# Optimization experiments

Hardware: AMD Instinct MI355X
Metric: run time of the kernel (lower is better)

## Reference

```python
import jax, jax.numpy as jnp
import numpy as np
import math

D_MODEL = 512
H = 8
DK = D_MODEL // H  # 64
DFF = 2048
EPS = 1e-5


def layernorm(x, g, b):
    mu = jnp.mean(x, axis=-1, keepdims=True)
    var = jnp.mean((x - mu) ** 2, axis=-1, keepdims=True)
    return (x - mu) * jax.lax.rsqrt(var + EPS) * g + b


def gelu(x):
    return jax.nn.gelu(x, approximate=False)  # torch nn.GELU default (erf)


def feedforward(x, W1, b1, lng, lnb, W2, b2):
    x1 = jnp.einsum('btd,df->btf', x, W1) + b1
    x1 = gelu(layernorm(x1, lng, lnb))
    return jnp.einsum('btf,fd->btd', x1, W2) + b2


def setup_inputs() -> dict:
    key = jax.random.key(0)
    ks = iter(jax.random.split(key, 32))
    s = 0.02
    d = {}
    d['x'] = jax.random.normal(next(ks), (4, 2048, D_MODEL), jnp.float32)
    # per-head QKV projections, stacked over heads: [H, d_model, dk]
    d['Wq'] = jax.random.normal(next(ks), (H, D_MODEL, DK), jnp.float32) * s
    d['bq'] = jnp.zeros((H, DK), jnp.float32)
    d['Wk'] = jax.random.normal(next(ks), (H, D_MODEL, DK), jnp.float32) * s
    d['bk'] = jnp.zeros((H, DK), jnp.float32)
    d['Wv'] = jax.random.normal(next(ks), (H, D_MODEL, DK), jnp.float32) * s
    d['bv'] = jnp.zeros((H, DK), jnp.float32)
    d['Wo'] = jax.random.normal(next(ks), (D_MODEL, D_MODEL), jnp.float32) * s
    d['bo'] = jnp.zeros((D_MODEL,), jnp.float32)
    d['ln1_g'] = jnp.ones((D_MODEL,), jnp.float32)
    d['ln1_b'] = jnp.zeros((D_MODEL,), jnp.float32)
    # main FFN
    d['ff_W1'] = jax.random.normal(next(ks), (D_MODEL, DFF), jnp.float32) * s
    d['ff_b1'] = jnp.zeros((DFF,), jnp.float32)
    d['ff_lng'] = jnp.ones((DFF,), jnp.float32)
    d['ff_lnb'] = jnp.zeros((DFF,), jnp.float32)
    d['ff_W2'] = jax.random.normal(next(ks), (DFF, D_MODEL), jnp.float32) * s
    d['ff_b2'] = jnp.zeros((D_MODEL,), jnp.float32)
    d['ln2_g'] = jnp.ones((D_MODEL,), jnp.float32)
    d['ln2_b'] = jnp.zeros((D_MODEL,), jnp.float32)
    d['alphaA'] = jnp.zeros((1,), jnp.float32) + 0.1
    d['alphaB'] = jnp.zeros((1,), jnp.float32) + 0.1
    d['p1'] = jnp.asarray(0.1, jnp.float32)
    # sub1 FFN
    d['s1_W1'] = jax.random.normal(next(ks), (D_MODEL, DFF), jnp.float32) * s
    d['s1_b1'] = jnp.zeros((DFF,), jnp.float32)
    d['s1_lng'] = jnp.ones((DFF,), jnp.float32)
    d['s1_lnb'] = jnp.zeros((DFF,), jnp.float32)
    d['s1_W2'] = jax.random.normal(next(ks), (DFF, D_MODEL), jnp.float32) * s
    d['s1_b2'] = jnp.zeros((D_MODEL,), jnp.float32)
    d['lnsub1_g'] = jnp.ones((D_MODEL,), jnp.float32)
    d['lnsub1_b'] = jnp.zeros((D_MODEL,), jnp.float32)
    d['p2'] = jnp.asarray(0.1, jnp.float32)
    d['sub2_W'] = jax.random.normal(next(ks), (D_MODEL, D_MODEL), jnp.float32) * s
    d['sub2_b'] = jnp.zeros((D_MODEL,), jnp.float32)
    d['lnsub2_g'] = jnp.ones((D_MODEL,), jnp.float32)
    d['lnsub2_b'] = jnp.zeros((D_MODEL,), jnp.float32)
    return d


def reference(x, Wq, bq, Wk, bk, Wv, bv, Wo, bo, ln1_g, ln1_b,
              ff_W1, ff_b1, ff_lng, ff_lnb, ff_W2, ff_b2, ln2_g, ln2_b,
              alphaA, alphaB, p1, s1_W1, s1_b1, s1_lng, s1_lnb, s1_W2, s1_b2,
              lnsub1_g, lnsub1_b, p2, sub2_W, sub2_b, lnsub2_g, lnsub2_b):
    # --- multi-head attention (q = k = v = x) ---
    q = jnp.einsum('btd,hdk->bhtk', x, Wq) + bq[:, None, :]
    k = jnp.einsum('btd,hdk->bhtk', x, Wk) + bk[:, None, :]
    v = jnp.einsum('btd,hdk->bhtk', x, Wv) + bv[:, None, :]
    scores = jnp.einsum('bhtk,bhsk->bhts', q, k) / math.sqrt(DK)
    probs = jax.nn.softmax(scores, axis=-1)
    heads = jnp.einsum('bhts,bhsv->bhtv', probs, v)           # [B,H,T,dv]
    B, _, T, _ = heads.shape
    cat = jnp.transpose(heads, (0, 2, 1, 3)).reshape(B, T, H * DK)
    attn = jnp.einsum('btd,de->bte', cat, Wo) + bo
    # --- residual stack ---
    ln1 = layernorm(x + attn, ln1_g, ln1_b)
    out1 = x + ln1 * alphaA
    fft = feedforward(out1, ff_W1, ff_b1, ff_lng, ff_lnb, ff_W2, ff_b2)
    ln2 = layernorm(fft + out1, ln2_g, ln2_b)
    out2 = out1 + ln2 * alphaB
    # --- sub-branch 1 ---
    sub1 = feedforward(x, s1_W1, s1_b1, s1_lng, s1_lnb, s1_W2, s1_b2)
    sub1 = p1 * gelu(layernorm(sub1, lnsub1_g, lnsub1_b))
    # --- sub-branch 2 ---
    sub2 = jnp.einsum('btd,de->bte', x, sub2_W) + sub2_b
    sub2 = p2 * gelu(layernorm(sub2, lnsub2_g, lnsub2_b))
    return out2 + sub1 + sub2
```

## Files before the change

kernel.cpp:

```cpp
#include <hip/hip_runtime.h>
#include <hip/hip_bf16.h>
#include <math.h>

typedef __hip_bfloat16 bf16;
typedef __attribute__((ext_vector_type(8))) short s8v;
typedef __attribute__((ext_vector_type(4))) float f4v;

#define T_SEQ 2048
#define ROWS 8192
#define DMODEL 512
#define DFF 2048
#define QS 2048

#define GL2LDS(g, l) __builtin_amdgcn_global_load_lds( \
    (const __attribute__((address_space(1))) void*)(g), \
    (__attribute__((address_space(3))) void*)(l), 16, 0, 0)

__device__ __forceinline__ float b2f(bf16 v) { return __bfloat162float(v); }
__device__ __forceinline__ bf16 f2b(float v) { return __float2bfloat16(v); }
__device__ __forceinline__ float us2f(unsigned short u) {
    union { float f; unsigned int u; } c; c.u = ((unsigned int)u) << 16; return c.f;
}
__device__ __forceinline__ unsigned short f2us(float v) {
    bf16 b = f2b(v); return *(unsigned short*)&b;
}
__device__ __forceinline__ float gelu_f(float x) {
    return 0.5f * x * (1.0f + erff(x * 0.70710678118654752440f));
}
__device__ __forceinline__ float ldP(const void* p, int i, bool f32) {
    return f32 ? ((const float*)p)[i] : b2f(((const bf16*)p)[i]);
}

__global__ __launch_bounds__(256) void sniff_kernel(const void* __restrict__ x,
                                                    int* __restrict__ flag) {
    __shared__ float red[4];
    int tid = threadIdx.x;
    const bf16* p = (const bf16*)x;
    float mx = 0.f;
    for (int i = tid; i < 65536; i += 256) {
        float v = b2f(p[i]);
        if (!(v == v)) v = 1e30f;
        mx = fmaxf(mx, fabsf(v));
    }
    #pragma unroll
    for (int o = 32; o; o >>= 1) mx = fmaxf(mx, __shfl_down(mx, o));
    if ((tid & 63) == 0) red[tid >> 6] = mx;
    __syncthreads();
    if (tid == 0) {
        float m = fmaxf(fmaxf(red[0], red[1]), fmaxf(red[2], red[3]));
        flag[0] = (m > 1000.f) ? 1 : 0;
    }
}

__global__ __launch_bounds__(256) void cvt_b16(const void* __restrict__ in,
                                               unsigned short* __restrict__ out, int n,
                                               const int* __restrict__ flag) {
    bool f32 = flag[0] != 0;
    int i = blockIdx.x * 256 + threadIdx.x;
    if (i < n) out[i] = f2us(ldP(in, i, f32));
}

#define WBIG_E 1048576
__global__ __launch_bounds__(256) void repack_all(const void* Wq, const void* Wk, const void* Wv,
                                                  const void* s2W, const void* ffW1, const void* ffW2,
                                                  const void* s1W1, const void* s1W2, const void* Wo,
                                                  unsigned short* __restrict__ Wbig,
                                                  unsigned short* __restrict__ ffW1t,
                                                  unsigned short* __restrict__ ffW2t,
                                                  unsigned short* __restrict__ s1W1t,
                                                  unsigned short* __restrict__ s1W2t,
                                                  unsigned short* __restrict__ Wot,
                                                  const int* __restrict__ flag) {
    bool f32 = flag[0] != 0;
    int idx = blockIdx.x * 256 + threadIdx.x;
    if (idx < WBIG_E) {
        int n = idx >> 9, d = idx & 511;
        float v;
        if (n < 1536) {
            int sec = n >> 9, nn = n & 511;
            int h = nn >> 6, j = nn & 63;
            const void* W = sec == 0 ? Wq : (sec == 1 ? Wk : Wv);
            v = ldP(W, (h * 512 + d) * 64 + j, f32);
        } else {
            v = ldP(s2W, d * 512 + (n - 1536), f32);
        }
        Wbig[idx] = f2us(v);
    } else if (idx < 2 * WBIG_E) {
        int i2 = idx - WBIG_E;
        int n = i2 >> 9, kd = i2 & 511;
        ffW1t[i2] = f2us(ldP(ffW1, kd * 2048 + n, f32));
    } else if (idx < 3 * WBIG_E) {
        int i2 = idx - 2 * WBIG_E;
        int n = i2 >> 11, kd = i2 & 2047;
        ffW2t[i2] = f2us(ldP(ffW2, kd * 512 + n, f32));
    } else if (idx < 4 * WBIG_E) {
        int i2 = idx - 3 * WBIG_E;
        int n = i2 >> 9, kd = i2 & 511;
        s1W1t[i2] = f2us(ldP(s1W1, kd * 2048 + n, f32));
    } else if (idx < 5 * WBIG_E) {
        int i2 = idx - 4 * WBIG_E;
        int n = i2 >> 11, kd = i2 & 2047;
        s1W2t[i2] = f2us(ldP(s1W2, kd * 512 + n, f32));
    } else if (idx < 5 * WBIG_E + 262144) {
        int i2 = idx - 5 * WBIG_E;
        int n = i2 >> 9, kd = i2 & 511;
        Wot[i2] = f2us(ldP(Wo, kd * 512 + n, f32));
    }
}

__global__ __launch_bounds__(256) void bias_fuse(const void* bq, const void* bk, const void* bv,
                                                 const void* s2b, const void* bo, const void* ffb1,
                                                 const void* ffb2, const void* s1b1, const void* s1b2,
                                                 float* __restrict__ out,
                                                 const int* __restrict__ flag) {
    bool f32 = flag[0] != 0;
    int i = blockIdx.x * 256 + threadIdx.x;
    if (i >= 7680) return;
    const void* src; int off;
    if      (i < 512)  { src = bq;   off = i; }
    else if (i < 1024) { src = bk;   off = i - 512; }
    else if (i < 1536) { src = bv;   off = i - 1024; }
    else if (i < 2048) { src = s2b;  off = i - 1536; }
    else if (i < 2560) { src = bo;   off = i - 2048; }
    else if (i < 4608) { src = ffb1; off = i - 2560; }
    else if (i < 5120) { src = ffb2; off = i - 4608; }
    else if (i < 7168) { src = s1b1; off = i - 5120; }
    else               { src = s1b2; off = i - 7168; }
    out[i] = ldP(src, off, f32);
}

__global__ __launch_bounds__(256) void gemm_mfma(const unsigned short* __restrict__ A,
                                                 const unsigned short* __restrict__ Bt,
                                                 const float* __restrict__ bias,
                                                 void* __restrict__ C0,
                                                 void* __restrict__ C1,
                                                 int M, int N, int K, int kLen,
                                                 int outBf16) {
    __shared__ unsigned short As[128 * 64];
    __shared__ unsigned short Bs[128 * 64];
    int tid = threadIdx.x;
    int wave = tid >> 6, lane = tid & 63;
    int wm = wave >> 1, wn = wave & 1;
    int quad = lane >> 4, l16 = lane & 15;
    int bm = blockIdx.y * 128, bn = blockIdx.x * 128;
    int z = blockIdx.z;
    int kOff = z * kLen;
    f4v acc[4][4] = {};
    int rsub = lane >> 3;
    int kcst = lane & 7;
    for (int k0 = kOff; k0 < kOff + kLen; k0 += 64) {
        #pragma unroll
        for (int i = 0; i < 4; i++) {
            int rowT = wave * 32 + i * 8 + rsub;
            int kc = (kcst - rowT) & 7;
            GL2LDS(A + (size_t)(bm + rowT) * K + k0 + kc * 8,
                   &As[(wave * 32 + i * 8) * 64]);
            GL2LDS(Bt + (size_t)(bn + rowT) * K + k0 + kc * 8,
                   &Bs[(wave * 32 + i * 8) * 64]);
        }
        __syncthreads();
        #pragma unroll
        for (int ks = 0; ks < 64; ks += 32) {
            int kchunk = (ks >> 3) + quad;
            s8v af[4], bfr[4];
            #pragma unroll
            for (int mi = 0; mi < 4; mi++) {
                int m = wm * 64 + mi * 16 + l16;
                af[mi] = *(const s8v*)&As[m * 64 + (((kchunk + m) & 7) * 8)];
            }
            #pragma unroll
            for (int ni = 0; ni < 4; ni++) {
                int n = wn * 64 + ni * 16 + l16;
                bfr[ni] = *(const s8v*)&Bs[n * 64 + (((kchunk + n) & 7) * 8)];
            }
            #pragma unroll
            for (int mi = 0; mi < 4; mi++)
                #pragma unroll
                for (int ni = 0; ni < 4; ni++)
                    acc[mi][ni] = __builtin_amdgcn_mfma_f32_16x16x32_bf16(
                        af[mi], bfr[ni], acc[mi][ni], 0, 0, 0);
        }
        __syncthreads();
    }
    bool doBias = (z == 0);
    float bcol[4];
    #pragma unroll
    for (int ni = 0; ni < 4; ni++)
        bcol[ni] = doBias ? bias[bn + wn * 64 + ni * 16 + l16] : 0.f;
    void* Cd = z ? C1 : C0;
    #pragma unroll
    for (int mi = 0; mi < 4; mi++) {
        #pragma unroll
        for (int rg = 0; rg < 4; rg++) {
            size_t row = bm + wm * 64 + mi * 16 + quad * 4 + rg;
            #pragma unroll
            for (int ni = 0; ni < 4; ni++) {
                int col = bn + wn * 64 + ni * 16 + l16;
                float v = acc[mi][ni][rg] + bcol[ni];
                if (outBf16) ((unsigned short*)Cd)[row * N + col] = f2us(v);
                else         ((float*)Cd)[row * N + col] = v;
            }
        }
    }
}

__global__ __launch_bounds__(256) void transpose_v(const unsigned short* __restrict__ QKV,
                                                   unsigned short* __restrict__ Vt) {
    __shared__ unsigned short tile[64][72];
    int kt = blockIdx.x;
    int bh = blockIdx.y;
    int b = bh >> 3, h = bh & 7;
    const unsigned short* Vg = QKV + ((size_t)b * T_SEQ) * QS + 1024 + h * 64;
    int tid = threadIdx.x;
    int r = tid >> 3, c = (tid & 7) * 8;
    #pragma unroll
    for (int it = 0; it < 2; it++) {
        int rr = r + it * 32;
        uint4 v = *(const uint4*)(Vg + (size_t)(kt * 64 + rr) * QS + c);
        *(uint4*)&tile[rr][c] = v;
    }
    __syncthreads();
    #pragma unroll
    for (int it = 0; it < 2; it++) {
        int d = r + it * 32;
        unsigned short tmp[8];
        #pragma unroll
        for (int j = 0; j < 8; j++) tmp[j] = tile[c + j][d];
        *(uint4*)(Vt + ((size_t)(bh * 64 + d)) * T_SEQ + kt * 64 + c) = *(uint4*)tmp;
    }
}

#define ALD 72
#define SCL2 0.18033688f
__global__ __launch_bounds__(256) void attn_mfma(const unsigned short* __restrict__ QKV,
                                                 const unsigned short* __restrict__ Vt,
                                                 unsigned short* __restrict__ O) {
    __shared__ unsigned short Qs[64 * ALD];
    __shared__ unsigned short Ks[64 * ALD];
    __shared__ unsigned short Vts[64 * ALD];
    __shared__ unsigned short Ps[64 * ALD];

    int tid = threadIdx.x;
    int wave = tid >> 6, lane = tid & 63;
    int quad = lane >> 4, l16 = lane & 15;
    int qbase = blockIdx.x * 64;
    int bh = blockIdx.y;
    int b = bh >> 3, h = bh & 7;
    const unsigned short* Qg = QKV + ((size_t)(b * T_SEQ + qbase)) * QS + h * 64;
    const unsigned short* Kg = QKV + ((size_t)b * T_SEQ) * QS + 512 + h * 64;
    const unsigned short* Vtg = Vt + (size_t)bh * 64 * T_SEQ;

    int r = tid >> 3, c = (tid & 7) * 8;
    #pragma unroll
    for (int it = 0; it < 2; it++) {
        int rr = r + it * 32;
        uint4 v = *(const uint4*)(Qg + (size_t)rr * QS + c);
        *(uint4*)&Qs[rr * ALD + c] = v;
    }
    float lrun[4] = {0.f, 0.f, 0.f, 0.f};
    f4v oacc[4] = {};
    __syncthreads();

    for (int kt = 0; kt < 32; ++kt) {
        #pragma unroll
        for (int it = 0; it < 2; it++) {
            int rr = r + it * 32;
            uint4 kv = *(const uint4*)(Kg + (size_t)(kt * 64 + rr) * QS + c);
            *(uint4*)&Ks[rr * ALD + c] = kv;
            uint4 vv = *(const uint4*)(Vtg + (size_t)rr * T_SEQ + kt * 64 + c);
            *(uint4*)&Vts[rr * ALD + c] = vv;
        }
        __syncthreads();

        f4v sacc[4] = {};
        #pragma unroll
        for (int kc2 = 0; kc2 < 2; kc2++) {
            s8v aq = *(const s8v*)&Qs[(wave * 16 + l16) * ALD + kc2 * 32 + quad * 8];
            #pragma unroll
            for (int ni = 0; ni < 4; ni++) {
                s8v bk_ = *(const s8v*)&Ks[(ni * 16 + l16) * ALD + kc2 * 32 + quad * 8];
                sacc[ni] = __builtin_amdgcn_mfma_f32_16x16x32_bf16(aq, bk_, sacc[ni], 0, 0, 0);
            }
        }
        #pragma unroll
        for (int rg = 0; rg < 4; rg++) {
            #pragma unroll
            for (int ni = 0; ni < 4; ni++) {
                float p = exp2f(fminf(sacc[ni][rg] * SCL2, 30.f));
                lrun[rg] += p;
                Ps[(wave * 16 + quad * 4 + rg) * ALD + ni * 16 + l16] = f2us(p);
            }
        }
        #pragma unroll
        for (int kc2 = 0; kc2 < 2; kc2++) {
            s8v ap = *(const s8v*)&Ps[(wave * 16 + l16) * ALD + kc2 * 32 + quad * 8];
            #pragma unroll
            for (int ni = 0; ni < 4; ni++) {
                s8v bv_ = *(const s8v*)&Vts[(ni * 16 + l16) * ALD + kc2 * 32 + quad * 8];
                oacc[ni] = __builtin_amdgcn_mfma_f32_16x16x32_bf16(ap, bv_, oacc[ni], 0, 0, 0);
            }
        }
        __syncthreads();
    }

    #pragma unroll
    for (int rg = 0; rg < 4; rg++) {
        float l = lrun[rg];
        #pragma unroll
        for (int o = 8; o; o >>= 1) l += __shfl_xor(l, o);
        float linv = 1.0f / l;
        size_t orow = ((size_t)(b * T_SEQ + qbase + wave * 16 + quad * 4 + rg)) * 512 + h * 64;
        #pragma unroll
        for (int ni = 0; ni < 4; ni++)
            O[orow + ni * 16 + l16] = f2us(oacc[ni][rg] * linv);
    }
}

__global__ __launch_bounds__(256) void ln_residual(const void* __restrict__ Xraw,
                                                   const float* __restrict__ Y,
                                                   const float* __restrict__ Y2,
                                                   const float* __restrict__ Xf,
                                                   const void* __restrict__ g,
                                                   const void* __restrict__ bb,
                                                   const void* __restrict__ alpha,
                                                   float* __restrict__ out,
                                                   unsigned short* __restrict__ outb,
                                                   const int* __restrict__ flag) {
    __shared__ float red[8];
    bool f32 = flag[0] != 0;
    int row = blockIdx.x, tid = threadIdx.x;
    size_t base = (size_t)row * DMODEL;
    float x0 = Xraw ? ldP(Xraw, base + tid, f32) : Xf[base + tid];
    float x1 = Xraw ? ldP(Xraw, base + tid + 256, f32) : Xf[base + tid + 256];
    float v0 = x0 + Y[base + tid];
    float v1 = x1 + Y[base + tid + 256];
    if (Y2) { v0 += Y2[base + tid]; v1 += Y2[base + tid + 256]; }
    float s = v0 + v1, s2 = v0 * v0 + v1 * v1;
    #pragma unroll
    for (int o = 32; o; o >>= 1) { s += __shfl_down(s, o); s2 += __shfl_down(s2, o); }
    if ((tid & 63) == 0) { red[tid >> 6] = s; red[4 + (tid >> 6)] = s2; }
    __syncthreads();
    s = red[0] + red[1] + red[2] + red[3];
    s2 = red[4] + red[5] + red[6] + red[7];
    float mu = s * (1.0f / 512.0f);
    float var = s2 * (1.0f / 512.0f) - mu * mu;
    float rr = rsqrtf(var + 1e-5f);
    float a = ldP(alpha, 0, f32);
    float o0 = x0 + a * ((v0 - mu) * rr * ldP(g, tid, f32) + ldP(bb, tid, f32));
    float o1 = x1 + a * ((v1 - mu) * rr * ldP(g, tid + 256, f32) + ldP(bb, tid + 256, f32));
    out[base + tid] = o0;
    out[base + tid + 256] = o1;
    if (outb) {
        outb[base + tid] = f2us(o0);
        outb[base + tid + 256] = f2us(o1);
    }
}

__global__ __launch_bounds__(256) void ln_gelu(unsigned short* __restrict__ Hm,
                                               const void* __restrict__ g,
                                               const void* __restrict__ bb,
                                               const int* __restrict__ flag) {
    __shared__ float red[8];
    bool f32 = flag[0] != 0;
    int row = blockIdx.x, tid = threadIdx.x;
    size_t base = (size_t)row * DFF;
    float v[8];
    float s = 0.f, s2 = 0.f;
    #pragma unroll
    for (int i = 0; i < 8; i++) {
        v[i] = us2f(Hm[base + tid + i * 256]);
        s += v[i]; s2 += v[i] * v[i];
    }
    #pragma unroll
    for (int o = 32; o; o >>= 1) { s += __shfl_down(s, o); s2 += __shfl_down(s2, o); }
    if ((tid & 63) == 0) { red[tid >> 6] = s; red[4 + (tid >> 6)] = s2; }
    __syncthreads();
    s = red[0] + red[1] + red[2] + red[3];
    s2 = red[4] + red[5] + red[6] + red[7];
    float mu = s * (1.0f / 2048.0f);
    float var = s2 * (1.0f / 2048.0f) - mu * mu;
    float r = rsqrtf(var + 1e-5f);
    #pragma unroll
    for (int i = 0; i < 8; i++) {
        int cc = tid + i * 256;
        float ln = (v[i] - mu) * r * ldP(g, cc, f32) + ldP(bb, cc, f32);
        Hm[base + cc] = f2us(gelu_f(ln));
    }
}

__global__ __launch_bounds__(256) void final_kernel(const float* __restrict__ O2,
                                                    const float* __restrict__ S1,
                                                    const float* __restrict__ S1b,
                                                    const unsigned short* __restrict__ S2,
                                                    const void* __restrict__ g1,
                                                    const void* __restrict__ b1,
                                                    const void* __restrict__ g2,
                                                    const void* __restrict__ b2,
                                                    const void* __restrict__ p1,
                                                    const void* __restrict__ p2,
                                                    void* __restrict__ out,
                                                    const int* __restrict__ flag) {
    __shared__ float red[16];
    bool f32 = flag[0] != 0;
    int row = blockIdx.x, tid = threadIdx.x;
    size_t base = (size_t)row * DMODEL;
    size_t base2 = (size_t)row * QS;
    float a0 = S1[base + tid] + S1b[base + tid];
    float a1 = S1[base + tid + 256] + S1b[base + tid + 256];
    float c0 = us2f(S2[base2 + tid]);
    float c1 = us2f(S2[base2 + tid + 256]);
    float sa = a0 + a1, sa2 = a0 * a0 + a1 * a1;
    float sc = c0 + c1, sc2 = c0 * c0 + c1 * c1;
    #pragma unroll
    for (int o = 32; o; o >>= 1) {
        sa += __shfl_down(sa, o); sa2 += __shfl_down(sa2, o);
        sc += __shfl_down(sc, o); sc2 += __shfl_down(sc2, o);
    }
    int w = tid >> 6;
    if ((tid & 63) == 0) { red[w] = sa; red[4 + w] = sa2; red[8 + w] = sc; red[12 + w] = sc2; }
    __syncthreads();
    sa = red[0] + red[1] + red[2] + red[3];
    sa2 = red[4] + red[5] + red[6] + red[7];
    sc = red[8] + red[9] + red[10] + red[11];
    sc2 = red[12] + red[13] + red[14] + red[15];
    float mua = sa * (1.0f / 512.0f), vara = sa2 * (1.0f / 512.0f) - mua * mua;
    float ra = rsqrtf(vara + 1e-5f);
    float muc = sc * (1.0f / 512.0f), varc = sc2 * (1.0f / 512.0f) - muc * muc;
    float rc = rsqrtf(varc + 1e-5f);
    float fp1 = ldP(p1, 0, f32), fp2 = ldP(p2, 0, f32);
    float av[2] = {a0, a1}, cv[2] = {c0, c1};
    #pragma unroll
    for (int i = 0; i < 2; i++) {
        int cc = tid + i * 256;
        float l1 = (av[i] - mua) * ra * ldP(g1, cc, f32) + ldP(b1, cc, f32);
        float l2 = (cv[i] - muc) * rc * ldP(g2, cc, f32) + ldP(b2, cc, f32);
        float o = O2[base + cc] + fp1 * gelu_f(l1) + fp2 * gelu_f(l2);
        if (f32) ((float*)out)[base + cc] = o;
        else     ((bf16*)out)[base + cc] = f2b(o);
    }
}

extern "C" void kernel_launch(void* const* d_in, const int* in_sizes, int n_in,
                              void* d_out, int out_size, void* d_ws, size_t ws_size,
                              hipStream_t stream) {
    (void)in_sizes; (void)n_in; (void)out_size; (void)ws_size;
    const void* x      = d_in[0];
    const void* Wq     = d_in[1];
    const void* bq     = d_in[2];
    const void* Wk     = d_in[3];
    const void* bk     = d_in[4];
    const void* Wv     = d_in[5];
    const void* bv     = d_in[6];
    const void* Wo     = d_in[7];
    const void* bo     = d_in[8];
    const void* ln1_g  = d_in[9];
    const void* ln1_b  = d_in[10];
    const void* ffW1   = d_in[11];
    const void* ffb1   = d_in[12];
    const void* fflng  = d_in[13];
    const void* fflnb  = d_in[14];
    const void* ffW2   = d_in[15];
    const void* ffb2   = d_in[16];
    const void* ln2_g  = d_in[17];
    const void* ln2_b  = d_in[18];
    const void* alphaA = d_in[19];
    const void* alphaB = d_in[20];
    const void* p1     = d_in[21];
    const void* s1W1   = d_in[22];
    const void* s1b1   = d_in[23];
    const void* s1lng  = d_in[24];
    const void* s1lnb  = d_in[25];
    const void* s1W2   = d_in[26];
    const void* s1b2   = d_in[27];
    const void* lns1g  = d_in[28];
    const void* lns1b  = d_in[29];
    const void* p2     = d_in[30];
    const void* s2W    = d_in[31];
    const void* s2b    = d_in[32];
    const void* lns2g  = d_in[33];
    const void* lns2b  = d_in[34];

    char* base = (char*)d_ws;
    size_t off = 0;
    auto alloc = [&](size_t bytes) {
        char* p = base + off;
        off += (bytes + 255) & ~(size_t)255;
        return p;
    };
    int* flag            = (int*)alloc(64);
    unsigned short* Wbig  = (unsigned short*)alloc((size_t)2048 * 512 * 2);
    unsigned short* Wot   = (unsigned short*)alloc(512 * 512 * 2);
    unsigned short* ffW1t = (unsigned short*)alloc((size_t)2048 * 512 * 2);
    unsigned short* ffW2t = (unsigned short*)alloc((size_t)512 * 2048 * 2);
    unsigned short* s1W1t = (unsigned short*)alloc((size_t)2048 * 512 * 2);
    unsigned short* s1W2t = (unsigned short*)alloc((size_t)512 * 2048 * 2);
    float* bias_all       = (float*)alloc(7680 * 4);
    unsigned short* xb    = (unsigned short*)alloc((size_t)ROWS * 512 * 2);
    unsigned short* Cbig  = (unsigned short*)alloc((size_t)ROWS * QS * 2);
    unsigned short* h1    = (unsigned short*)alloc((size_t)ROWS * DFF * 2);
    unsigned short* Vtb   = (unsigned short*)alloc((size_t)ROWS * 512 * 2);
    char*  regionC        = alloc((size_t)ROWS * 512 * 2);
    char*  regionB        = alloc((size_t)ROWS * 512 * 4);
    char*  regionD        = alloc((size_t)ROWS * 512 * 4);
    float* out2           = (float*)alloc((size_t)ROWS * 512 * 4);

    float* attn           = (float*)regionB;
    float* fft            = (float*)regionB;
    float* sub1raw2       = (float*)regionB;
    unsigned short* catb  = (unsigned short*)regionC;
    unsigned short* out1b = (unsigned short*)regionC;
    float* out1           = (float*)regionD;
    float* sub1raw        = (float*)regionD;
    float* attn2          = out2;
    float* fft2           = out2;

    float* biasBig = bias_all + 0;
    float* biasWo  = bias_all + 2048;
    float* biasF1  = bias_all + 2560;
    float* biasF2  = bias_all + 4608;
    float* biasS11 = bias_all + 5120;
    float* biasS12 = bias_all + 7168;

    sniff_kernel<<<1, 256, 0, stream>>>(x, flag);
    cvt_b16<<<(ROWS * 512 + 255) / 256, 256, 0, stream>>>(x, xb, ROWS * 512, flag);
    repack_all<<<(5 * WBIG_E + 262144 + 255) / 256, 256, 0, stream>>>(
        Wq, Wk, Wv, s2W, ffW1, ffW2, s1W1, s1W2, Wo,
        Wbig, ffW1t, ffW2t, s1W1t, s1W2t, Wot, flag);
    bias_fuse<<<30, 256, 0, stream>>>(bq, bk, bv, s2b, bo, ffb1, ffb2, s1b1, s1b2,
                                      bias_all, flag);

    auto gemm = [&](const unsigned short* A, const unsigned short* Bt, const float* bias,
                    void* C0, void* C1, int M, int N, int K, int outBf16, int split) {
        int kLen = split ? K / 2 : K;
        gemm_mfma<<<dim3(N / 128, M / 128, split ? 2 : 1), 256, 0, stream>>>(
            A, Bt, bias, C0, C1, M, N, K, kLen, outBf16);
    };

    gemm(xb, Wbig, biasBig, Cbig, nullptr, ROWS, QS, 512, 1, 0);
    transpose_v<<<dim3(32, 32), 256, 0, stream>>>(Cbig, Vtb);
    attn_mfma<<<dim3(T_SEQ / 64, 32), 256, 0, stream>>>(Cbig, Vtb, catb);
    gemm(catb, Wot, biasWo, attn, attn2, ROWS, 512, 512, 0, 1);
    ln_residual<<<ROWS, 256, 0, stream>>>(x, attn, attn2, nullptr,
                                          ln1_g, ln1_b, alphaA, out1, out1b, flag);
    gemm(out1b, ffW1t, biasF1, h1, nullptr, ROWS, DFF, 512, 1, 0);
    ln_gelu<<<ROWS, 256, 0, stream>>>(h1, fflng, fflnb, flag);
    gemm(h1, ffW2t, biasF2, fft, fft2, ROWS, 512, DFF, 0, 1);
    ln_residual<<<ROWS, 256, 0, stream>>>(nullptr, fft, fft2, out1,
                                          ln2_g, ln2_b, alphaB, out2,
                                          (unsigned short*)nullptr, flag);
    gemm(xb, s1W1t, biasS11, h1, nullptr, ROWS, DFF, 512, 1, 0);
    ln_gelu<<<ROWS, 256, 0, stream>>>(h1, s1lng, s1lnb, flag);
    gemm(h1, s1W2t, biasS12, sub1raw, sub1raw2, ROWS, 512, DFF, 0, 1);
    final_kernel<<<ROWS, 256, 0, stream>>>(out2, sub1raw, sub1raw2, Cbig + 1536,
                                           lns1g, lns1b, lns2g, lns2b,
                                           p1, p2, d_out, flag);
}
```

Measured before the change: 559.6 us.

## Fuse sub1 first-layer GEMM into QKV projection and store split-K partials as bf16

The sub-branch-1 first FFN weight is appended to the big QKV+sub2 weight, so one wider GEMM over x produces Q, K, V, sub2 and the sub1 hidden activations together. The GEMM gains lda/ldc strides so later GEMMs and ln_gelu can read and write the hidden slice inside the wide buffer in place. The sub1 branch is then processed early, the attention-output and sub1 split-K partials are written as bf16 instead of fp32, and buffers are re-aliased. The aim is fewer launches, better GEMM occupancy and less memory traffic, at the cost of extra bf16 rounding in the partial sums and more complex buffer aliasing.

After: 558.8 us. Within noise of the previous version (-0.2%).

```diff
diff --git a/kernel.cpp b/kernel.cpp
--- a/kernel.cpp
+++ b/kernel.cpp
@@ -10,7 +10,7 @@
 #define ROWS 8192
 #define DMODEL 512
 #define DFF 2048
-#define QS 2048
+#define QS 4096
 
 #define GL2LDS(g, l) __builtin_amdgcn_global_load_lds( \
     (const __attribute__((address_space(1))) void*)(g), \
@@ -60,20 +60,19 @@
     if (i < n) out[i] = f2us(ldP(in, i, f32));
 }
 
-#define WBIG_E 1048576
 __global__ __launch_bounds__(256) void repack_all(const void* Wq, const void* Wk, const void* Wv,
-                                                  const void* s2W, const void* ffW1, const void* ffW2,
-                                                  const void* s1W1, const void* s1W2, const void* Wo,
-                                                  unsigned short* __restrict__ Wbig,
+                                                  const void* s2W, const void* s1W1,
+                                                  const void* ffW1, const void* ffW2,
+                                                  const void* s1W2, const void* Wo,
+                                                  unsigned short* __restrict__ Wbig2,
                                                   unsigned short* __restrict__ ffW1t,
                                                   unsigned short* __restrict__ ffW2t,
-                                                  unsigned short* __restrict__ s1W1t,
                                                   unsigned short* __restrict__ s1W2t,
                                                   unsigned short* __restrict__ Wot,
                                                   const int* __restrict__ flag) {
     bool f32 = flag[0] != 0;
     int idx = blockIdx.x * 256 + threadIdx.x;
-    if (idx < WBIG_E) {
+    if (idx < 2097152) {
         int n = idx >> 9, d = idx & 511;
         float v;
         if (n < 1536) {
@@ -81,36 +80,34 @@
             int h = nn >> 6, j = nn & 63;
             const void* W = sec == 0 ? Wq : (sec == 1 ? Wk : Wv);
             v = ldP(W, (h * 512 + d) * 64 + j, f32);
+        } else if (n < 2048) {
+            v = ldP(s2W, d * 512 + (n - 1536), f32);
         } else {
-            v = ldP(s2W, d * 512 + (n - 1536), f32);
-        }
-        Wbig[idx] = f2us(v);
-    } else if (idx < 2 * WBIG_E) {
-        int i2 = idx - WBIG_E;
+            v = ldP(s1W1, d * 2048 + (n - 2048), f32);
+        }
+        Wbig2[idx] = f2us(v);
+    } else if (idx < 3145728) {
+        int i2 = idx - 2097152;
         int n = i2 >> 9, kd = i2 & 511;
         ffW1t[i2] = f2us(ldP(ffW1, kd * 2048 + n, f32));
-    } else if (idx < 3 * WBIG_E) {
-        int i2 = idx - 2 * WBIG_E;
+    } else if (idx < 4194304) {
+        int i2 = idx - 3145728;
         int n = i2 >> 11, kd = i2 & 2047;
         ffW2t[i2] = f2us(ldP(ffW2, kd * 512 + n, f32));
-    } else if (idx < 4 * WBIG_E) {
-        int i2 = idx - 3 * WBIG_E;
-        int n = i2 >> 9, kd = i2 & 511;
-        s1W1t[i2] = f2us(ldP(s1W1, kd * 2048 + n, f32));
-    } else if (idx < 5 * WBIG_E) {
-        int i2 = idx - 4 * WBIG_E;
+    } else if (idx < 5242880) {
+        int i2 = idx - 4194304;
         int n = i2 >> 11, kd = i2 & 2047;
         s1W2t[i2] = f2us(ldP(s1W2, kd * 512 + n, f32));
-    } else if (idx < 5 * WBIG_E + 262144) {
-        int i2 = idx - 5 * WBIG_E;
+    } else if (idx < 5505024) {
+        int i2 = idx - 5242880;
         int n = i2 >> 9, kd = i2 & 511;
         Wot[i2] = f2us(ldP(Wo, kd * 512 + n, f32));
     }
 }
 
 __global__ __launch_bounds__(256) void bias_fuse(const void* bq, const void* bk, const void* bv,
-                                                 const void* s2b, const void* bo, const void* ffb1,
-                                                 const void* ffb2, const void* s1b1, const void* s1b2,
+                                                 const void* s2b, const void* s1b1, const void* bo,
+                                                 const void* ffb1, const void* ffb2, const void* s1b2,
                                                  float* __restrict__ out,
                                                  const int* __restrict__ flag) {
     bool f32 = flag[0] != 0;
@@ -121,20 +118,20 @@
     else if (i < 1024) { src = bk;   off = i - 512; }
     else if (i < 1536) { src = bv;   off = i - 1024; }
     else if (i < 2048) { src = s2b;  off = i - 1536; }
-    else if (i < 2560) { src = bo;   off = i - 2048; }
-    else if (i < 4608) { src = ffb1; off = i - 2560; }
-    else if (i < 5120) { src = ffb2; off = i - 4608; }
-    else if (i < 7168) { src = s1b1; off = i - 5120; }
+    else if (i < 4096) { src = s1b1; off = i - 2048; }
+    else if (i < 4608) { src = bo;   off = i - 4096; }
+    else if (i < 6656) { src = ffb1; off = i - 4608; }
+    else if (i < 7168) { src = ffb2; off = i - 6656; }
     else               { src = s1b2; off = i - 7168; }
     out[i] = ldP(src, off, f32);
 }
 
-__global__ __launch_bounds__(256) void gemm_mfma(const unsigned short* __restrict__ A,
+__global__ __launch_bounds__(256) void gemm_mfma(const unsigned short* __restrict__ A, int lda,
                                                  const unsigned short* __restrict__ Bt,
                                                  const float* __restrict__ bias,
                                                  void* __restrict__ C0,
                                                  void* __restrict__ C1,
-                                                 int M, int N, int K, int kLen,
+                                                 int M, int N, int ldc, int K, int kLen,
                                                  int outBf16) {
     __shared__ unsigned short As[128 * 64];
     __shared__ unsigned short Bs[128 * 64];
@@ -153,7 +150,7 @@
         for (int i = 0; i < 4; i++) {
             int rowT = wave * 32 + i * 8 + rsub;
             int kc = (kcst - rowT) & 7;
-            GL2LDS(A + (size_t)(bm + rowT) * K + k0 + kc * 8,
+            GL2LDS(A + (size_t)(bm + rowT) * lda + k0 + kc * 8,
                    &As[(wave * 32 + i * 8) * 64]);
             GL2LDS(Bt + (size_t)(bn + rowT) * K + k0 + kc * 8,
                    &Bs[(wave * 32 + i * 8) * 64]);
@@ -197,8 +194,8 @@
             for (int ni = 0; ni < 4; ni++) {
                 int col = bn + wn * 64 + ni * 16 + l16;
                 float v = acc[mi][ni][rg] + bcol[ni];
-                if (outBf16) ((unsigned short*)Cd)[row * N + col] = f2us(v);
-                else         ((float*)Cd)[row * N + col] = v;
+                if (outBf16) ((unsigned short*)Cd)[row * ldc + col] = f2us(v);
+                else         ((float*)Cd)[row * ldc + col] = v;
             }
         }
     }
@@ -316,25 +313,23 @@
     }
 }
 
-__global__ __launch_bounds__(256) void ln_residual(const void* __restrict__ Xraw,
-                                                   const float* __restrict__ Y,
-                                                   const float* __restrict__ Y2,
-                                                   const float* __restrict__ Xf,
-                                                   const void* __restrict__ g,
-                                                   const void* __restrict__ bb,
-                                                   const void* __restrict__ alpha,
-                                                   float* __restrict__ out,
-                                                   unsigned short* __restrict__ outb,
-                                                   const int* __restrict__ flag) {
+__global__ __launch_bounds__(256) void ln_res1(const void* __restrict__ Xraw,
+                                               const unsigned short* __restrict__ Ya,
+                                               const unsigned short* __restrict__ Yb,
+                                               const void* __restrict__ g,
+                                               const void* __restrict__ bb,
+                                               const void* __restrict__ alpha,
+                                               float* __restrict__ out,
+                                               unsigned short* __restrict__ outb,
+                                               const int* __restrict__ flag) {
     __shared__ float red[8];
     bool f32 = flag[0] != 0;
     int row = blockIdx.x, tid = threadIdx.x;
     size_t base = (size_t)row * DMODEL;
-    float x0 = Xraw ? ldP(Xraw, base + tid, f32) : Xf[base + tid];
-    float x1 = Xraw ? ldP(Xraw, base + tid + 256, f32) : Xf[base + tid + 256];
-    float v0 = x0 + Y[base + tid];
-    float v1 = x1 + Y[base + tid + 256];
-    if (Y2) { v0 += Y2[base + tid]; v1 += Y2[base + tid + 256]; }
+    float x0 = ldP(Xraw, base + tid, f32);
+    float x1 = ldP(Xraw, base + tid + 256, f32);
+    float v0 = x0 + us2f(Ya[base + tid]) + us2f(Yb[base + tid]);
+    float v1 = x1 + us2f(Ya[base + tid + 256]) + us2f(Yb[base + tid + 256]);
     float s = v0 + v1, s2 = v0 * v0 + v1 * v1;
     #pragma unroll
     for (int o = 32; o; o >>= 1) { s += __shfl_down(s, o); s2 += __shfl_down(s2, o); }
@@ -350,20 +345,48 @@
     float o1 = x1 + a * ((v1 - mu) * rr * ldP(g, tid + 256, f32) + ldP(bb, tid + 256, f32));
     out[base + tid] = o0;
     out[base + tid + 256] = o1;
-    if (outb) {
-        outb[base + tid] = f2us(o0);
-        outb[base + tid + 256] = f2us(o1);
-    }
-}
-
-__global__ __launch_bounds__(256) void ln_gelu(unsigned short* __restrict__ Hm,
+    outb[base + tid] = f2us(o0);
+    outb[base + tid + 256] = f2us(o1);
+}
+
+__global__ __launch_bounds__(256) void ln_res2(const float* __restrict__ Xf,
+                                               const float* __restrict__ Y,
+                                               const float* __restrict__ Y2,
+                                               const void* __restrict__ g,
+                                               const void* __restrict__ bb,
+                                               const void* __restrict__ alpha,
+                                               float* __restrict__ out,
+                                               const int* __restrict__ flag) {
+    __shared__ float red[8];
+    bool f32 = flag[0] != 0;
+    int row = blockIdx.x, tid = threadIdx.x;
+    size_t base = (size_t)row * DMODEL;
+    float x0 = Xf[base + tid], x1 = Xf[base + tid + 256];
+    float v0 = x0 + Y[base + tid] + Y2[base + tid];
+    float v1 = x1 + Y[base + tid + 256] + Y2[base + tid + 256];
+    float s = v0 + v1, s2 = v0 * v0 + v1 * v1;
+    #pragma unroll
+    for (int o = 32; o; o >>= 1) { s += __shfl_down(s, o); s2 += __shfl_down(s2, o); }
+    if ((tid & 63) == 0) { red[tid >> 6] = s; red[4 + (tid >> 6)] = s2; }
+    __syncthreads();
+    s = red[0] + red[1] + red[2] + red[3];
+    s2 = red[4] + red[5] + red[6] + red[7];
+    float mu = s * (1.0f / 512.0f);
+    float var = s2 * (1.0f / 512.0f) - mu * mu;
+    float rr = rsqrtf(var + 1e-5f);
+    float a = ldP(alpha, 0, f32);
+    out[base + tid] = x0 + a * ((v0 - mu) * rr * ldP(g, tid, f32) + ldP(bb, tid, f32));
+    out[base + tid + 256] = x1 + a * ((v1 - mu) * rr * ldP(g, tid + 256, f32) + ldP(bb, tid + 256, f32));
+}
+
+__global__ __launch_bounds__(256) void ln_gelu(unsigned short* __restrict__ Hm, int stride,
                                                const void* __restrict__ g,
                                                const void* __restrict__ bb,
                                                const int* __restrict__ flag) {
     __shared__ float red[8];
     bool f32 = flag[0] != 0;
     int row = blockIdx.x, tid = threadIdx.x;
-    size_t base = (size_t)row * DFF;
+    size_t base = (size_t)row * stride;
     float v[8];
     float s = 0.f, s2 = 0.f;
     #pragma unroll
@@ -389,8 +412,8 @@
 }
 
 __global__ __launch_bounds__(256) void final_kernel(const float* __restrict__ O2,
-                                                    const float* __restrict__ S1,
-                                                    const float* __restrict__ S1b,
+                                                    const unsigned short* __restrict__ S1,
+                                                    const unsigned short* __restrict__ S1b,
                                                     const unsigned short* __restrict__ S2,
                                                     const void* __restrict__ g1,
                                                     const void* __restrict__ b1,
@@ -405,8 +428,8 @@
     int row = blockIdx.x, tid = threadIdx.x;
     size_t base = (size_t)row * DMODEL;
     size_t base2 = (size_t)row * QS;
-    float a0 = S1[base + tid] + S1b[base + tid];
-    float a1 = S1[base + tid + 256] + S1b[base + tid + 256];
+    float a0 = us2f(S1[base + tid]) + us2f(S1b[base + tid]);
+    float a1 = us2f(S1[base + tid + 256]) + us2f(S1b[base + tid + 256]);
     float c0 = us2f(S2[base2 + tid]);
     float c1 = us2f(S2[base2 + tid + 256]);
     float sa = a0 + a1, sa2 = a0 * a0 + a1 * a1;
@@ -487,71 +510,68 @@
         off += (bytes + 255) & ~(size_t)255;
         return p;
     };
-    int* flag            = (int*)alloc(64);
-    unsigned short* Wbig  = (unsigned short*)alloc((size_t)2048 * 512 * 2);
-    unsigned short* Wot   = (unsigned short*)alloc(512 * 512 * 2);
+    int* flag             = (int*)alloc(256);
+    unsigned short* Wbig2 = (unsigned short*)alloc((size_t)4096 * 512 * 2);
     unsigned short* ffW1t = (unsigned short*)alloc((size_t)2048 * 512 * 2);
     unsigned short* ffW2t = (unsigned short*)alloc((size_t)512 * 2048 * 2);
-    unsigned short* s1W1t = (unsigned short*)alloc((size_t)2048 * 512 * 2);
     unsigned short* s1W2t = (unsigned short*)alloc((size_t)512 * 2048 * 2);
+    unsigned short* Wot   = (unsigned short*)alloc(512 * 512 * 2);
     float* bias_all       = (float*)alloc(7680 * 4);
-    unsigned short* xb    = (unsigned short*)alloc((size_t)ROWS * 512 * 2);
-    unsigned short* Cbig  = (unsigned short*)alloc((size_t)ROWS * QS * 2);
-    unsigned short* h1    = (unsigned short*)alloc((size_t)ROWS * DFF * 2);
-    unsigned short* Vtb   = (unsigned short*)alloc((size_t)ROWS * 512 * 2);
-    char*  regionC        = alloc((size_t)ROWS * 512 * 2);
-    char*  regionB        = alloc((size_t)ROWS * 512 * 4);
-    char*  regionD        = alloc((size_t)ROWS * 512 * 4);
-    float* out2           = (float*)alloc((size_t)ROWS * 512 * 4);
-
-    float* attn           = (float*)regionB;
-    float* fft            = (float*)regionB;
-    float* sub1raw2       = (float*)regionB;
-    unsigned short* catb  = (unsigned short*)regionC;
-    unsigned short* out1b = (unsigned short*)regionC;
-    float* out1           = (float*)regionD;
-    float* sub1raw        = (float*)regionD;
-    float* attn2          = out2;
-    float* fft2           = out2;
+    char*  regX           = alloc((size_t)ROWS * 512 * 2);
+    char*  regCat         = alloc((size_t)ROWS * 512 * 2);
+    unsigned short* Cbig2 = (unsigned short*)alloc((size_t)ROWS * QS * 2);
+    char*  regB           = alloc((size_t)ROWS * 512 * 2);
+    char*  regD           = alloc((size_t)ROWS * 512 * 2);
+    float* out1           = (float*)alloc((size_t)ROWS * 512 * 4);
+    char*  regO           = alloc((size_t)ROWS * 512 * 4);
+
+    unsigned short* xb    = (unsigned short*)regX;
+    unsigned short* Vtb   = (unsigned short*)regX;
+    unsigned short* out1b = (unsigned short*)regX;
+    unsigned short* catb  = (unsigned short*)regCat;
+    float* fft            = (float*)regX;
+    unsigned short* sub1raw  = (unsigned short*)regB;
+    unsigned short* sub1raw2 = (unsigned short*)regD;
+    unsigned short* attnA = (unsigned short*)regO;
+    unsigned short* attnB = (unsigned short*)(regO + (size_t)ROWS * 512 * 2);
+    float* fft2           = (float*)regO;
+    float* out2           = (float*)regO;
 
     float* biasBig = bias_all + 0;
-    float* biasWo  = bias_all + 2048;
-    float* biasF1  = bias_all + 2560;
-    float* biasF2  = bias_all + 4608;
-    float* biasS11 = bias_all + 5120;
+    float* biasWo  = bias_all + 4096;
+    float* biasF1  = bias_all + 4608;
+    float* biasF2  = bias_all + 6656;
     float* biasS12 = bias_all + 7168;
 
     sniff_kernel<<<1, 256, 0, stream>>>(x, flag);
     cvt_b16<<<(ROWS * 512 + 255) / 256, 256, 0, stream>>>(x, xb, ROWS * 512, flag);
-    repack_all<<<(5 * WBIG_E + 262144 + 255) / 256, 256, 0, stream>>>(
-        Wq, Wk, Wv, s2W, ffW1, ffW2, s1W1, s1W2, Wo,
-        Wbig, ffW1t, ffW2t, s1W1t, s1W2t, Wot, flag);
-    bias_fuse<<<30, 256, 0, stream>>>(bq, bk, bv, s2b, bo, ffb1, ffb2, s1b1, s1b2,
+    repack_all<<<(5505024 + 255) / 256, 256, 0, stream>>>(
+        Wq, Wk, Wv, s2W, s1W1, ffW1, ffW2, s1W2, Wo,
+        Wbig2, ffW1t, ffW2t, s1W2t, Wot, flag);
+    bias_fuse<<<30, 256, 0, stream>>>(bq, bk, bv, s2b, s1b1, bo, ffb1, ffb2, s1b2,
                                       bias_all, flag);
 
-    auto gemm = [&](const unsigned short* A, const unsigned short* Bt, const float* bias,
-                    void* C0, void* C1, int M, int N, int K, int outBf16, int split) {
+    auto gemm = [&](const unsigned short* A, int lda, const unsigned short* Bt,
+                    const float* bias, void* C0, void* C1,
+                    int M, int N, int ldc, int K, int outBf16, int split) {
         int kLen = split ? K / 2 : K;
         gemm_mfma<<<dim3(N / 128, M / 128, split ? 2 : 1), 256, 0, stream>>>(
-            A, Bt, bias, C0, C1, M, N, K, kLen, outBf16);
+            A, lda, Bt, bias, C0, C1, M, N, ldc, K, kLen, outBf16);
     };
 
-    gemm(xb, Wbig, biasBig, Cbig, nullptr, ROWS, QS, 512, 1, 0);
-    transpose_v<<<dim3(32, 32), 256, 0, stream>>>(Cbig, Vtb);
-    attn_mfma<<<dim3(T_SEQ / 64, 32), 256, 0, stream>>>(Cbig, Vtb, catb);
-    gemm(catb, Wot, biasWo, attn, attn2, ROWS, 512, 512, 0, 1);
-    ln_residual<<<ROWS, 256, 0, stream>>>(x, attn, attn2, nullptr,
-                                          ln1_g, ln1_b, alphaA, out1, out1b, flag);
-    gemm(out1b, ffW1t, biasF1, h1, nullptr, ROWS, DFF, 512, 1, 0);
-    ln_gelu<<<ROWS, 256, 0, stream>>>(h1, fflng, fflnb, flag);
-    gemm(h1, ffW2t, biasF2, fft, fft2, ROWS, 512, DFF, 0, 1);
-    ln_residual<<<ROWS, 256, 0, stream>>>(nullptr, fft, fft2, out1,
-                                          ln2_g, ln2_b, alphaB, out2,
-                                          (unsigned short*)nullptr, flag);
-    gemm(xb, s1W1t, biasS11, h1, nullptr, ROWS, DFF, 512, 1, 0);
-    ln_gelu<<<ROWS, 256, 0, stream>>>(h1, s1lng, s1lnb, flag);
-    gemm(h1, s1W2t, biasS12, sub1raw, sub1raw2, ROWS, 512, DFF, 0, 1);
-    final_kernel<<<ROWS, 256, 0, stream>>>(out2, sub1raw, sub1raw2, Cbig + 1536,
+    gemm(xb, 512, Wbig2, biasBig, Cbig2, nullptr, ROWS, 4096, 4096, 512, 1, 0);
+    transpose_v<<<dim3(32, 32), 256, 0, stream>>>(Cbig2, Vtb);
+    attn_mfma<<<dim3(T_SEQ / 64, 32), 256, 0, stream>>>(Cbig2, Vtb, catb);
+    ln_gelu<<<ROWS, 256, 0, stream>>>(Cbig2 + 2048, QS, s1lng, s1lnb, flag);
+    gemm(Cbig2 + 2048, QS, s1W2t, biasS12, sub1raw, sub1raw2, ROWS, 512, 512, 2048, 1, 1);
+    gemm(catb, 512, Wot, biasWo, attnA, attnB, ROWS, 512, 512, 512, 1, 1);
+    ln_res1<<<ROWS, 256, 0, stream>>>(x, attnA, attnB, ln1_g, ln1_b, alphaA,
+                                      out1, out1b, flag);
+    gemm(out1b, 512, ffW1t, biasF1, Cbig2 + 2048, nullptr, ROWS, 2048, 4096, 512, 1, 0);
+    ln_gelu<<<ROWS, 256, 0, stream>>>(Cbig2 + 2048, QS, fflng, fflnb, flag);
+    gemm(Cbig2 + 2048, QS, ffW2t, biasF2, fft, fft2, ROWS, 512, 512, 2048, 0, 1);
+    ln_res2<<<ROWS, 256, 0, stream>>>(out1, fft, fft2, ln2_g, ln2_b, alphaB, out2, flag);
+    final_kernel<<<ROWS, 256, 0, stream>>>(out2, sub1raw, sub1raw2, Cbig2 + 1536,
                                            lns1g, lns1b, lns2g, lns2b,
                                            p1, p2, d_out, flag);
 }
```
